# Performance work log

Measured on AMD Instinct MI355X. Metric: run time of the kernel, lower is better.

The kernel has to match this reference:

```python
import jax, jax.numpy as jnp
import numpy as np

GROUPS = 8
EPS = 1e-5
PERM_IN = {'x': (0, 2, 4, 1, 3), 'y': (0, 2, 3, 1, 4), 'seq': (0, 3, 4, 1, 2)}
PERM_OUT = {'x': (0, 3, 1, 4, 2), 'y': (0, 3, 1, 2, 4), 'seq': (0, 3, 4, 1, 2)}


def bn_train(x, gamma, beta, axis=1):
    """Training-mode batch norm: normalize over all axes except `axis`."""
    axes = tuple(i for i in range(x.ndim) if i != axis)
    mean = x.mean(axes, keepdims=True)
    var = x.var(axes, keepdims=True)
    shp = [1] * x.ndim
    shp[axis] = x.shape[axis]
    return (x - mean) * jax.lax.rsqrt(var + EPS) * gamma.reshape(shp) + beta.reshape(shp)


def axial_attn(x, qkv_w, gq, bq, gs, bs, go, bo, direction):
    # x: (N, C, seq, H, W)
    x = jnp.transpose(x, PERM_IN[direction])
    N, seq, W, C, H = x.shape
    B = N * seq * W
    xf = x.reshape(B, C, H)
    # 1x1 conv1d qkv projection + BN over channels
    qkv = jnp.einsum('oc,bch->boh', qkv_w, xf)            # (B, 2C, H)
    qkv = bn_train(qkv, gq, bq, axis=1)
    gp = C // GROUPS                                       # group_planes
    qkv = qkv.reshape(B, GROUPS, 2 * gp, H)
    q = qkv[:, :, : gp // 2]
    k = qkv[:, :, gp // 2: gp]
    v = qkv[:, :, gp:]
    qk = jnp.einsum('bgci,bgcj->bgij', q, k)               # (B, g, H, H)
    qk = bn_train(qk, gs, bs, axis=1)
    sim = jax.nn.softmax(qk, axis=3)
    sv = jnp.einsum('bgij,bgcj->bgci', sim, v)             # (B, g, gp, H)
    sv = bn_train(sv.reshape(B, C, H), go, bo, axis=1)
    out = sv.reshape(N, seq, W, C, H)
    return jnp.transpose(out, PERM_OUT[direction])


def setup_inputs() -> dict:
    key = jax.random.key(0)
    ks = jax.random.split(key, 4)
    N, C_in, seq, H, W = 2, 128, 16, 56, 56
    width = 64
    x = jax.random.normal(ks[0], (N, C_in, seq, H, W), jnp.float32)
    cd_w = jax.random.normal(ks[1], (width, C_in), jnp.float32) * (1.0 / np.sqrt(C_in))
    qkv_w = jax.random.normal(ks[2], (3, 2 * width, width), jnp.float32) * (1.0 / np.sqrt(width))
    cu_w = jax.random.normal(ks[3], (2 * width, width), jnp.float32) * (1.0 / np.sqrt(width))
    return {
        'x': x,
        'cd_w': cd_w,
        'bn1_g': jnp.ones((width,), jnp.float32),
        'bn1_b': jnp.zeros((width,), jnp.float32),
        'qkv_w': qkv_w,
        'bnq_g': jnp.ones((3, 2 * width), jnp.float32),
        'bnq_b': jnp.zeros((3, 2 * width), jnp.float32),
        'bns_g': jnp.ones((3, GROUPS), jnp.float32),
        'bns_b': jnp.zeros((3, GROUPS), jnp.float32),
        'bno_g': jnp.ones((3, width), jnp.float32),
        'bno_b': jnp.zeros((3, width), jnp.float32),
        'cu_w': cu_w,
        'bn2_g': jnp.ones((2 * width,), jnp.float32),
        'bn2_b': jnp.zeros((2 * width,), jnp.float32),
    }


def reference(x, cd_w, bn1_g, bn1_b, qkv_w, bnq_g, bnq_b, bns_g, bns_b,
              bno_g, bno_b, cu_w, bn2_g, bn2_b):
    identity = x
    out = jnp.einsum('oc,ncshw->noshw', cd_w, x)           # conv_down (1x1)
    out = jax.nn.relu(bn_train(out, bn1_g, bn1_b, axis=1))
    for i, d in enumerate(('x', 'y', 'seq')):              # height, width, seq axial passes
        out = axial_attn(out, qkv_w[i], bnq_g[i], bnq_b[i], bns_g[i], bns_b[i],
                         bno_g[i], bno_b[i], d)
    out = jax.nn.relu(out)
    out = jnp.einsum('oc,ncshw->noshw', cu_w, out)         # conv_up (1x1)
    out = bn_train(out, bn2_g, bn2_b, axis=1)
    return jax.nn.relu(out + identity)
```

## Files before the change

### kernel.cpp

```cpp
#include <hip/hip_runtime.h>

constexpr int SP = 16*56*56;
constexpr int P  = 2*SP;
constexpr float EPSV = 1e-5f;

constexpr size_t SZ_A   = (size_t)2*64*SP;
constexpr size_t OFF_A  = 0;
constexpr size_t OFF_C  = SZ_A;
constexpr size_t OFF_ST = OFF_C + SZ_A;
constexpr size_t OFF_P1 = 0;
constexpr size_t OFF_P2 = 65536;

__global__ void __launch_bounds__(256) kern_down(
    const float* __restrict__ x, const float* __restrict__ w,
    float* __restrict__ A, float* __restrict__ st)
{
  __shared__ float xs[128*64];
  __shared__ float wt[64*129];
  __shared__ float ssum[64], ssq[64];
  const int t = threadIdx.x;
  if (t < 64) { ssum[t] = 0.f; ssq[t] = 0.f; }
  const int p0 = blockIdx.x * 64;
  const int n = p0 / SP, rem = p0 % SP;
  const float* xb = x + (size_t)n*128*SP + rem;
  for (int e = t; e < 128*64; e += 256) {
    int c = e >> 6, p = e & 63;
    xs[e] = xb[(size_t)c*SP + p];
  }
  for (int e = t; e < 64*128; e += 256) {
    int o = e >> 7, c = e & 127;
    wt[o*129 + c] = w[e];
  }
  __syncthreads();
  const int og = t & 15, pg = t >> 4;
  float acc[4][4] = {};
  for (int c = 0; c < 128; ++c) {
    float xv[4], wv[4];
    #pragma unroll
    for (int j = 0; j < 4; ++j) xv[j] = xs[c*64 + pg*4 + j];
    #pragma unroll
    for (int i = 0; i < 4; ++i) wv[i] = wt[(og + 16*i)*129 + c];
    #pragma unroll
    for (int i = 0; i < 4; ++i) {
      #pragma unroll
      for (int j = 0; j < 4; ++j) acc[i][j] = fmaf(wv[i], xv[j], acc[i][j]);
    }
  }
  float* Ab = A + (size_t)n*64*SP + rem;
  #pragma unroll
  for (int i = 0; i < 4; ++i) {
    const int o = og + 16*i;
    float s1 = 0.f, s2 = 0.f;
    #pragma unroll
    for (int j = 0; j < 4; ++j) { float v = acc[i][j]; s1 += v; s2 += v*v; }
    float4 v4 = make_float4(acc[i][0], acc[i][1], acc[i][2], acc[i][3]);
    *reinterpret_cast<float4*>(Ab + (size_t)o*SP + pg*4) = v4;
    atomicAdd(&ssum[o], s1);
    atomicAdd(&ssq[o], s2);
  }
  __syncthreads();
  if (t < 64) { atomicAdd(&st[t], ssum[t]); atomicAdd(&st[64+t], ssq[t]); }
}

__global__ void __launch_bounds__(256) kern_up(
    const float* __restrict__ A, const float* __restrict__ w,
    float* __restrict__ U, float* __restrict__ st)
{
  __shared__ float xs[64*64];
  __shared__ float wt[128*65];
  __shared__ float ssum[128], ssq[128];
  const int t = threadIdx.x;
  if (t < 128) { ssum[t]=0.f; ssq[t]=0.f; }
  const int p0 = blockIdx.x*64;
  const int n = p0/SP, rem = p0%SP;
  const float* Ab = A + (size_t)n*64*SP + rem;
  for (int e = t; e < 64*64; e += 256) {
    int c = e >> 6, p = e & 63;
    xs[e] = fmaxf(Ab[(size_t)c*SP + p], 0.f);
  }
  for (int e = t; e < 128*64; e += 256) {
    int o = e >> 6, c = e & 63;
    wt[o*65 + c] = w[e];
  }
  __syncthreads();
  const int og = t & 31, pg = t >> 5;
  float acc[4][8] = {};
  for (int c = 0; c < 64; ++c) {
    float xv[8];
    #pragma unroll
    for (int j = 0; j < 8; ++j) xv[j] = xs[c*64 + pg*8 + j];
    #pragma unroll
    for (int i = 0; i < 4; ++i) {
      float wv = wt[(og + 32*i)*65 + c];
      #pragma unroll
      for (int j = 0; j < 8; ++j) acc[i][j] = fmaf(wv, xv[j], acc[i][j]);
    }
  }
  float* Ub = U + (size_t)n*128*SP + rem;
  #pragma unroll
  for (int i = 0; i < 4; ++i) {
    const int o = og + 32*i;
    float s1=0.f, s2=0.f;
    #pragma unroll
    for (int j = 0; j < 8; ++j) { float v = acc[i][j]; s1 += v; s2 += v*v; }
    float4 a = make_float4(acc[i][0],acc[i][1],acc[i][2],acc[i][3]);
    float4 b = make_float4(acc[i][4],acc[i][5],acc[i][6],acc[i][7]);
    *reinterpret_cast<float4*>(Ub + (size_t)o*SP + pg*8)     = a;
    *reinterpret_cast<float4*>(Ub + (size_t)o*SP + pg*8 + 4) = b;
    atomicAdd(&ssum[o], s1); atomicAdd(&ssq[o], s2);
  }
  __syncthreads();
  if (t < 128) { atomicAdd(&st[t], ssum[t]); atomicAdd(&st[128+t], ssq[t]); }
}

template<int DIR, bool FIRST>
__global__ void __launch_bounds__(256) kern_qkv(
    const float* __restrict__ A, const float* __restrict__ w,
    const float* __restrict__ sc1, const float* __restrict__ sh1,
    float* __restrict__ Bq, float* __restrict__ st)
{
  constexpr int H = 56;
  constexpr int SHJ = H/8;
  __shared__ float xs[64*H];
  __shared__ float wt[128*65];
  __shared__ float ssum[128], ssq[128];
  const int t = threadIdx.x;
  if (t < 128) { ssum[t]=0.f; ssq[t]=0.f; }
  const int b = blockIdx.x;
  size_t base; int strT;
  if (DIR == 0)      { int n=b/896,  r=b%896,  s=r/56, ww=r%56; base=(size_t)n*64*SP + s*3136 + ww;    strT=56;   }
  else               { int n=b/896,  r=b%896,  s=r/56, y=r%56;  base=(size_t)n*64*SP + s*3136 + y*56;  strT=1;    }
  for (int e = t; e < 64*H; e += 256) {
    int c = e / H, j = e % H;
    float v = A[base + (size_t)c*SP + (size_t)j*strT];
    if (FIRST) v = fmaxf(fmaf(v, sc1[c], sh1[c]), 0.f);
    xs[e] = v;
  }
  for (int e = t; e < 128*64; e += 256) { int o=e>>6, c=e&63; wt[o*65+c]=w[e]; }
  __syncthreads();
  const int og = t & 31, hg = t >> 5;
  float acc[4][SHJ];
  #pragma unroll
  for (int i=0;i<4;++i) {
    #pragma unroll
    for (int j=0;j<SHJ;++j) acc[i][j]=0.f;
  }
  for (int c = 0; c < 64; ++c) {
    float xv[SHJ];
    #pragma unroll
    for (int j = 0; j < SHJ; ++j) xv[j] = xs[c*H + hg*SHJ + j];
    #pragma unroll
    for (int i = 0; i < 4; ++i) {
      float wv = wt[(og + 32*i)*65 + c];
      #pragma unroll
      for (int j = 0; j < SHJ; ++j) acc[i][j] = fmaf(wv, xv[j], acc[i][j]);
    }
  }
  float* ob = Bq + (size_t)b*128*H;
  #pragma unroll
  for (int i = 0; i < 4; ++i) {
    const int o = og + 32*i;
    float s1=0.f, s2=0.f;
    #pragma unroll
    for (int j = 0; j < SHJ; ++j) {
      float v = acc[i][j];
      ob[o*H + hg*SHJ + j] = v;
      s1 += v; s2 += v*v;
    }
    atomicAdd(&ssum[o], s1); atomicAdd(&ssq[o], s2);
  }
  __syncthreads();
  if (t < 128) { atomicAdd(&st[t], ssum[t]); atomicAdd(&st[128+t], ssq[t]); }
}

__global__ void __launch_bounds__(256) kern_qkv2(
    const float* __restrict__ A, const float* __restrict__ w,
    float* __restrict__ Bq, float* __restrict__ st)
{
  __shared__ float xs[64*64];
  __shared__ float wt[128*65];
  __shared__ float ssum[128], ssq[128];
  const int t = threadIdx.x;
  if (t < 128) { ssum[t]=0.f; ssq[t]=0.f; }
  const int b = blockIdx.x;
  const int n = b/784, r = b%784, y = r/14, w4 = (r%14)*4;
  const float* Ab = A + (size_t)n*64*SP + y*56 + w4;
  for (int e = t; e < 1024; e += 256) {
    int c = e >> 4, s = e & 15;
    float4 v = *reinterpret_cast<const float4*>(Ab + (size_t)c*SP + s*3136);
    xs[c*64 + s]      = v.x;
    xs[c*64 + 16 + s] = v.y;
    xs[c*64 + 32 + s] = v.z;
    xs[c*64 + 48 + s] = v.w;
  }
  for (int e = t; e < 128*64; e += 256) { int o=e>>6, c=e&63; wt[o*65+c]=w[e]; }
  __syncthreads();
  const int og = t & 31, cg = t >> 5;
  float acc[4][8] = {};
  for (int c = 0; c < 64; ++c) {
    float xv[8];
    #pragma unroll
    for (int j = 0; j < 8; ++j) xv[j] = xs[c*64 + cg*8 + j];
    #pragma unroll
    for (int i = 0; i < 4; ++i) {
      float wv = wt[(og + 32*i)*65 + c];
      #pragma unroll
      for (int j = 0; j < 8; ++j) acc[i][j] = fmaf(wv, xv[j], acc[i][j]);
    }
  }
  const size_t b0 = (size_t)n*3136 + (size_t)y*56 + w4;
  #pragma unroll
  for (int i = 0; i < 4; ++i) {
    const int o = og + 32*i;
    float s1=0.f, s2=0.f;
    #pragma unroll
    for (int j = 0; j < 8; ++j) {
      int col = cg*8 + j, wl = col >> 4, s = col & 15;
      float v = acc[i][j];
      Bq[(b0 + wl)*2048 + o*16 + s] = v;
      s1 += v; s2 += v*v;
    }
    atomicAdd(&ssum[o], s1); atomicAdd(&ssq[o], s2);
  }
  __syncthreads();
  if (t < 128) { atomicAdd(&st[t], ssum[t]); atomicAdd(&st[128+t], ssq[t]); }
}

__global__ void __launch_bounds__(256) kern_red(
    const float* __restrict__ part, float* __restrict__ stout, int nb, int stride)
{
  const int ch = blockIdx.x;
  float s = 0.f;
  for (int i = threadIdx.x; i < nb; i += 256) s += part[(size_t)i*stride + ch];
  #pragma unroll
  for (int off = 32; off >= 1; off >>= 1) s += __shfl_xor(s, off);
  __shared__ float red[4];
  if ((threadIdx.x & 63) == 0) red[threadIdx.x >> 6] = s;
  __syncthreads();
  if (threadIdx.x == 0) stout[ch] = red[0] + red[1] + red[2] + red[3];
}

template<int H>
__global__ void __launch_bounds__(256) kern_pass1(
    const float* __restrict__ Bq, const float* __restrict__ qsc,
    const float* __restrict__ qsh, float* __restrict__ part)
{
  constexpr int PW = (H==16) ? 4 : 1;
  const int t = threadIdx.x;
  const int wave = t >> 6, lane = t & 63;
  const int sub = (PW==1) ? 0 : (lane >> 4);
  const int i = (PW==1) ? lane : (lane & 15);
  __shared__ float kls[4][4*H*PW];
  __shared__ float bs[16];
  if (t < 16) bs[t] = 0.f;
  float* klw = kls[wave];
  const int pair0 = (blockIdx.x*4 + wave)*PW;
  for (int e = lane; e < 4*H*PW; e += 64) {
    int sp = e / (4*H), r = e % (4*H);
    int c = r / H, j = r % H;
    int pr = pair0 + sp, bb = pr >> 3, g = pr & 7;
    int o = g*16 + 4 + c;
    klw[e] = fmaf(Bq[((size_t)bb*128 + o)*H + j], qsc[o], qsh[o]);
  }
  __syncthreads();
  const int pr = pair0 + sub, bb = pr >> 3, g = pr & 7;
  const float* kp = klw + sub*4*H;
  const bool act = (i < H);
  float q[4];
  #pragma unroll
  for (int c = 0; c < 4; ++c) {
    int o = g*16 + c;
    q[c] = act ? fmaf(Bq[((size_t)bb*128 + o)*H + i], qsc[o], qsh[o]) : 0.f;
  }
  float s1 = 0.f, s2 = 0.f;
  #pragma unroll
  for (int j = 0; j < H; ++j) {
    float s = q[0]*kp[j] + q[1]*kp[H+j] + q[2]*kp[2*H+j] + q[3]*kp[3*H+j];
    s1 += s; s2 += s*s;
  }
  #pragma unroll
  for (int off = (PW==1?32:8); off >= 1; off >>= 1) {
    s1 += __shfl_xor(s1, off);
    s2 += __shfl_xor(s2, off);
  }
  if ((lane & (PW==1?63:15)) == 0) { atomicAdd(&bs[g], s1); atomicAdd(&bs[8+g], s2); }
  __syncthreads();
  if (t < 16) part[(size_t)blockIdx.x*16 + t] = bs[t];
}

template<int H>
__global__ void __launch_bounds__(256) kern_attn(
    const float* __restrict__ Bq, const float* __restrict__ qsc,
    const float* __restrict__ qsh, const float* __restrict__ ssc,
    float* __restrict__ C, float* __restrict__ part)
{
  constexpr int PW = (H==16) ? 4 : 1;
  const int t = threadIdx.x;
  const int wave = t >> 6, lane = t & 63;
  const int sub = (PW==1) ? 0 : (lane >> 4);
  const int i = (PW==1) ? lane : (lane & 15);
  __shared__ float kv[4][12*H*PW];
  __shared__ float bsum[64], bsq[64];
  if (t < 64) { bsum[t] = 0.f; bsq[t] = 0.f; }
  float* kvw = kv[wave];
  const int pair0 = (blockIdx.x*4 + wave)*PW;
  for (int e = lane; e < 12*H*PW; e += 64) {
    int sp = e / (12*H), r = e % (12*H);
    int c = r / H, j = r % H;
    int pr = pair0 + sp, bb = pr >> 3, g = pr & 7;
    int o = g*16 + 4 + c;
    kvw[e] = fmaf(Bq[((size_t)bb*128 + o)*H + j], qsc[o], qsh[o]);
  }
  __syncthreads();
  const int pr = pair0 + sub, bb = pr >> 3, g = pr & 7;
  const float* kp = kvw + sub*12*H;
  const bool act = (i < H);
  float q[4];
  #pragma unroll
  for (int c = 0; c < 4; ++c) {
    int o = g*16 + c;
    q[c] = act ? fmaf(Bq[((size_t)bb*128 + o)*H + i], qsc[o], qsh[o]) : 0.f;
  }
  const float As = ssc[g];
  float m = -3.4e38f;
  for (int j = 0; j < H; ++j) {
    float s = As * (q[0]*kp[j] + q[1]*kp[H+j] + q[2]*kp[2*H+j] + q[3]*kp[3*H+j]);
    m = fmaxf(m, s);
  }
  float den = 0.f;
  float acc[8] = {};
  for (int j = 0; j < H; ++j) {
    float s = As * (q[0]*kp[j] + q[1]*kp[H+j] + q[2]*kp[2*H+j] + q[3]*kp[3*H+j]);
    float e = __expf(s - m);
    den += e;
    #pragma unroll
    for (int c = 0; c < 8; ++c) acc[c] = fmaf(e, kp[(4+c)*H + j], acc[c]);
  }
  const float inv = 1.f/den;
  #pragma unroll
  for (int c = 0; c < 8; ++c) {
    float vv = act ? acc[c]*inv : 0.f;
    if (act) C[((size_t)bb*64 + g*8 + c)*H + i] = vv;
    float s1 = vv, s2 = vv*vv;
    #pragma unroll
    for (int off = (PW==1?32:8); off >= 1; off >>= 1) {
      s1 += __shfl_xor(s1, off);
      s2 += __shfl_xor(s2, off);
    }
    if ((lane & (PW==1?63:15)) == 0) { atomicAdd(&bsum[g*8+c], s1); atomicAdd(&bsq[g*8+c], s2); }
  }
  __syncthreads();
  if (t < 64) {
    part[(size_t)blockIdx.x*128 + t]      = bsum[t];
    part[(size_t)blockIdx.x*128 + 64 + t] = bsq[t];
  }
}

__global__ void __launch_bounds__(256) kern_scat0(
    const float* __restrict__ C, const float* __restrict__ osc,
    const float* __restrict__ osh, float* __restrict__ A)
{
  __shared__ float tile[56*57];
  const int bid = blockIdx.x;
  const int c = bid & 63, s = (bid >> 6) & 15, n = bid >> 10;
  const float sc = osc[c], sh = osh[c];
  const size_t cb = ((size_t)(n*16+s)*56)*3584 + c*56;
  for (int e = threadIdx.x; e < 3136; e += 256) {
    int w = e/56, h = e%56;
    tile[w*57+h] = C[cb + (size_t)w*3584 + h];
  }
  __syncthreads();
  const size_t ab = ((size_t)(n*64+c)*16+s)*3136;
  for (int e = threadIdx.x; e < 3136; e += 256) {
    int h = e/56, w = e%56;
    A[ab + e] = fmaf(tile[w*57+h], sc, sh);
  }
}

__global__ void __launch_bounds__(256) kern_scat1(
    const float* __restrict__ C, const float* __restrict__ osc,
    const float* __restrict__ osh, float* __restrict__ A)
{
  const int e = blockIdx.x*256 + threadIdx.x;
  if (e >= 1792*64*56) return;
  const int w = e % 56, c = (e/56) & 63, b = e / (56*64);
  const int n = b/896, r = b%896, s = r/56, y = r%56;
  A[((size_t)(n*64+c)*16+s)*3136 + y*56 + w] = fmaf(C[e], osc[c], osh[c]);
}

__global__ void __launch_bounds__(256) kern_scat2(
    const float* __restrict__ C, const float* __restrict__ osc,
    const float* __restrict__ osh, float* __restrict__ A)
{
  __shared__ float tile[56*17];
  const int bid = blockIdx.x;
  const int y = bid % 56, c = (bid/56) & 63, n = bid / 3584;
  const float sc = osc[c], sh = osh[c];
  const size_t cb = ((size_t)(n*56+y)*56)*1024 + c*16;
  for (int e = threadIdx.x; e < 896; e += 256) {
    int w = e >> 4, s = e & 15;
    tile[w*17+s] = C[cb + (size_t)w*1024 + s];
  }
  __syncthreads();
  const size_t ab = (size_t)(n*64+c)*16*3136 + y*56;
  for (int e = threadIdx.x; e < 896; e += 256) {
    int s = e/56, w = e%56;
    A[ab + (size_t)s*3136 + w] = fmaf(tile[w*17+s], sc, sh);
  }
}

__global__ void kern_fin_bn(float* __restrict__ st, const float* __restrict__ g,
                            const float* __restrict__ b, int nch, float invc)
{
  const int t = threadIdx.x;
  if (t < nch) {
    float mean = st[t]*invc;
    float var  = st[nch+t]*invc - mean*mean;
    float sc   = g[t]*rsqrtf(var + EPSV);
    st[2*nch+t] = sc;
    st[3*nch+t] = b[t] - mean*sc;
  }
}

__global__ void __launch_bounds__(256) kern_final(
    float* __restrict__ U, const float* __restrict__ x,
    const float* __restrict__ sc, const float* __restrict__ sh,
    float* __restrict__ out)
{
  const int idx = blockIdx.x*256 + threadIdx.x;
  if (idx >= P*128/4) return;
  const int e = idx*4;
  const int o = (e / SP) & 127;
  float4 u  = *reinterpret_cast<const float4*>(U + e);
  float4 xv = *reinterpret_cast<const float4*>(x + e);
  const float s = sc[o], h = sh[o];
  float4 r;
  r.x = fmaxf(fmaf(u.x, s, h) + xv.x, 0.f);
  r.y = fmaxf(fmaf(u.y, s, h) + xv.y, 0.f);
  r.z = fmaxf(fmaf(u.z, s, h) + xv.z, 0.f);
  r.w = fmaxf(fmaf(u.w, s, h) + xv.w, 0.f);
  *reinterpret_cast<float4*>(out + e) = r;
}

extern "C" void kernel_launch(void* const* d_in, const int* in_sizes, int n_in,
                              void* d_out, int out_size, void* d_ws, size_t ws_size,
                              hipStream_t stream)
{
  const float* x    = (const float*)d_in[0];
  const float* cdw  = (const float*)d_in[1];
  const float* bn1g = (const float*)d_in[2];
  const float* bn1b = (const float*)d_in[3];
  const float* qkvw = (const float*)d_in[4];
  const float* bnqg = (const float*)d_in[5];
  const float* bnqb = (const float*)d_in[6];
  const float* bnsg = (const float*)d_in[7];
  const float* bnsb = (const float*)d_in[8];
  const float* bnog = (const float*)d_in[9];
  const float* bnob = (const float*)d_in[10];
  const float* cuw  = (const float*)d_in[11];
  const float* bn2g = (const float*)d_in[12];
  const float* bn2b = (const float*)d_in[13];
  float* out = (float*)d_out;
  float* ws  = (float*)d_ws;

  float* A   = ws + OFF_A;
  float* C   = ws + OFF_C;
  float* st  = ws + OFF_ST;
  float* Pp1 = ws + OFF_P1;
  float* Pp2 = ws + OFF_P2;
  float* Bq  = out;

  hipMemsetAsync(st, 0, 4096*sizeof(float), stream);

  const float invP = 1.f/100352.f;

  kern_down<<<P/64, 256, 0, stream>>>(x, cdw, A, st);
  kern_fin_bn<<<1, 128, 0, stream>>>(st, bn1g, bn1b, 64, invP);

  {
    float* stq = st + 256; float* sts = stq + 512; float* sto = stq + 544;
    kern_qkv<0,true><<<1792, 256, 0, stream>>>(A, qkvw, st+128, st+192, Bq, stq);
    kern_fin_bn<<<1, 128, 0, stream>>>(stq, bnqg, bnqb, 128, invP);
    kern_pass1<56><<<3584, 256, 0, stream>>>(Bq, stq+256, stq+384, Pp1);
    kern_red<<<16, 256, 0, stream>>>(Pp1, sts, 3584, 16);
    kern_fin_bn<<<1, 128, 0, stream>>>(sts, bnsg, bnsb, 8, 1.f/5619712.f);
    kern_attn<56><<<3584, 256, 0, stream>>>(Bq, stq+256, stq+384, sts+16, C, Pp2);
    kern_red<<<128, 256, 0, stream>>>(Pp2, sto, 3584, 128);
    kern_fin_bn<<<1, 128, 0, stream>>>(sto, bnog, bnob, 64, invP);
    kern_scat0<<<2048, 256, 0, stream>>>(C, sto+128, sto+192, A);
  }
  {
    float* stq = st + 256 + 1024; float* sts = stq + 512; float* sto = stq + 544;
    kern_qkv<1,false><<<1792, 256, 0, stream>>>(A, qkvw+8192, st, st, Bq, stq);
    kern_fin_bn<<<1, 128, 0, stream>>>(stq, bnqg+128, bnqb+128, 128, invP);
    kern_pass1<56><<<3584, 256, 0, stream>>>(Bq, stq+256, stq+384, Pp1);
    kern_red<<<16, 256, 0, stream>>>(Pp1, sts, 3584, 16);
    kern_fin_bn<<<1, 128, 0, stream>>>(sts, bnsg+8, bnsb+8, 8, 1.f/5619712.f);
    kern_attn<56><<<3584, 256, 0, stream>>>(Bq, stq+256, stq+384, sts+16, C, Pp2);
    kern_red<<<128, 256, 0, stream>>>(Pp2, sto, 3584, 128);
    kern_fin_bn<<<1, 128, 0, stream>>>(sto, bnog+64, bnob+64, 64, invP);
    kern_scat1<<<25088, 256, 0, stream>>>(C, sto+128, sto+192, A);
  }
  {
    float* stq = st + 256 + 2048; float* sts = stq + 512; float* sto = stq + 544;
    kern_qkv2<<<1568, 256, 0, stream>>>(A, qkvw+16384, Bq, stq);
    kern_fin_bn<<<1, 128, 0, stream>>>(stq, bnqg+256, bnqb+256, 128, invP);
    kern_pass1<16><<<3136, 256, 0, stream>>>(Bq, stq+256, stq+384, Pp1);
    kern_red<<<16, 256, 0, stream>>>(Pp1, sts, 3136, 16);
    kern_fin_bn<<<1, 128, 0, stream>>>(sts, bnsg+16, bnsb+16, 8, 1.f/1605632.f);
    kern_attn<16><<<3136, 256, 0, stream>>>(Bq, stq+256, stq+384, sts+16, C, Pp2);
    kern_red<<<128, 256, 0, stream>>>(Pp2, sto, 3136, 128);
    kern_fin_bn<<<1, 128, 0, stream>>>(sto, bnog+128, bnob+128, 64, invP);
    kern_scat2<<<7168, 256, 0, stream>>>(C, sto+128, sto+192, A);
  }

  float* st2 = st + 3328;
  kern_up<<<P/64, 256, 0, stream>>>(A, cuw, Bq, st2);
  kern_fin_bn<<<1, 128, 0, stream>>>(st2, bn2g, bn2b, 128, invP);
  kern_final<<<P*128/4/256, 256, 0, stream>>>(Bq, x, st2+256, st2+384, out);
}
```

Before: 667.1 us.

## Vectorize tile loads, pre-transpose x-pass input, fuse partial reduce with BN finalize

Global-to-shared loads in the down, up and qkv kernels now use float4 instead of scalar loads. For the first axial pass, a new transpose kernel rewrites A so each H/W plane is transposed, which lets one qkv kernel read contiguous rows instead of strided columns. The separate partial-sum reduction and BN finalize launches are merged into one kernel that writes scale and shift directly, removing several small launches. The cost is an extra full read and write of A for the transpose, and it relies on C being free as scratch at that point.

```diff
diff --git a/kernel.cpp b/kernel.cpp
--- a/kernel.cpp
+++ b/kernel.cpp
@@ -23,13 +23,15 @@
   const int p0 = blockIdx.x * 64;
   const int n = p0 / SP, rem = p0 % SP;
   const float* xb = x + (size_t)n*128*SP + rem;
-  for (int e = t; e < 128*64; e += 256) {
-    int c = e >> 6, p = e & 63;
-    xs[e] = xb[(size_t)c*SP + p];
-  }
-  for (int e = t; e < 64*128; e += 256) {
-    int o = e >> 7, c = e & 127;
-    wt[o*129 + c] = w[e];
+  for (int e4 = t; e4 < 128*16; e4 += 256) {
+    int c = e4 >> 4, p4 = (e4 & 15)*4;
+    float4 v = *reinterpret_cast<const float4*>(xb + (size_t)c*SP + p4);
+    *reinterpret_cast<float4*>(&xs[c*64 + p4]) = v;
+  }
+  for (int e4 = t; e4 < 64*32; e4 += 256) {
+    int o = e4 >> 5, c4 = (e4 & 31)*4;
+    float4 v = *reinterpret_cast<const float4*>(w + o*128 + c4);
+    *reinterpret_cast<float4*>(&wt[o*129 + c4]) = v;
   }
   __syncthreads();
   const int og = t & 15, pg = t >> 4;
@@ -62,6 +64,25 @@
   if (t < 64) { atomicAdd(&st[t], ssum[t]); atomicAdd(&st[64+t], ssq[t]); }
 }
 
+__global__ void __launch_bounds__(256) kern_tr(
+    const float* __restrict__ A, float* __restrict__ At)
+{
+  __shared__ float tile[56*57];
+  const size_t base = (size_t)blockIdx.x*3136;
+  for (int e4 = threadIdx.x; e4 < 784; e4 += 256) {
+    int e = e4*4, h = e/56, w = e%56;
+    float4 v = *reinterpret_cast<const float4*>(A + base + e);
+    tile[w*57+h] = v.x; tile[(w+1)*57+h] = v.y;
+    tile[(w+2)*57+h] = v.z; tile[(w+3)*57+h] = v.w;
+  }
+  __syncthreads();
+  for (int e4 = threadIdx.x; e4 < 784; e4 += 256) {
+    int e = e4*4, w = e/56, h = e%56;
+    float4 v = make_float4(tile[w*57+h], tile[w*57+h+1], tile[w*57+h+2], tile[w*57+h+3]);
+    *reinterpret_cast<float4*>(At + base + e) = v;
+  }
+}
+
 __global__ void __launch_bounds__(256) kern_up(
     const float* __restrict__ A, const float* __restrict__ w,
     float* __restrict__ U, float* __restrict__ st)
@@ -74,13 +95,16 @@
   const int p0 = blockIdx.x*64;
   const int n = p0/SP, rem = p0%SP;
   const float* Ab = A + (size_t)n*64*SP + rem;
-  for (int e = t; e < 64*64; e += 256) {
-    int c = e >> 6, p = e & 63;
-    xs[e] = fmaxf(Ab[(size_t)c*SP + p], 0.f);
-  }
-  for (int e = t; e < 128*64; e += 256) {
-    int o = e >> 6, c = e & 63;
-    wt[o*65 + c] = w[e];
+  for (int e4 = t; e4 < 64*16; e4 += 256) {
+    int c = e4 >> 4, p4 = (e4 & 15)*4;
+    float4 v = *reinterpret_cast<const float4*>(Ab + (size_t)c*SP + p4);
+    v.x = fmaxf(v.x, 0.f); v.y = fmaxf(v.y, 0.f); v.z = fmaxf(v.z, 0.f); v.w = fmaxf(v.w, 0.f);
+    *reinterpret_cast<float4*>(&xs[c*64 + p4]) = v;
+  }
+  for (int e4 = t; e4 < 128*16; e4 += 256) {
+    int o = e4 >> 4, c4 = (e4 & 15)*4;
+    float4 v = *reinterpret_cast<const float4*>(w + o*64 + c4);
+    *reinterpret_cast<float4*>(&wt[o*65 + c4]) = v;
   }
   __syncthreads();
   const int og = t & 31, pg = t >> 5;
@@ -113,47 +137,49 @@
   if (t < 128) { atomicAdd(&st[t], ssum[t]); atomicAdd(&st[128+t], ssq[t]); }
 }
 
-template<int DIR, bool FIRST>
+template<bool FIRST>
 __global__ void __launch_bounds__(256) kern_qkv(
-    const float* __restrict__ A, const float* __restrict__ w,
+    const float* __restrict__ src, const float* __restrict__ w,
     const float* __restrict__ sc1, const float* __restrict__ sh1,
     float* __restrict__ Bq, float* __restrict__ st)
 {
   constexpr int H = 56;
-  constexpr int SHJ = H/8;
   __shared__ float xs[64*H];
   __shared__ float wt[128*65];
   __shared__ float ssum[128], ssq[128];
   const int t = threadIdx.x;
   if (t < 128) { ssum[t]=0.f; ssq[t]=0.f; }
   const int b = blockIdx.x;
-  size_t base; int strT;
-  if (DIR == 0)      { int n=b/896,  r=b%896,  s=r/56, ww=r%56; base=(size_t)n*64*SP + s*3136 + ww;    strT=56;   }
-  else               { int n=b/896,  r=b%896,  s=r/56, y=r%56;  base=(size_t)n*64*SP + s*3136 + y*56;  strT=1;    }
-  for (int e = t; e < 64*H; e += 256) {
-    int c = e / H, j = e % H;
-    float v = A[base + (size_t)c*SP + (size_t)j*strT];
-    if (FIRST) v = fmaxf(fmaf(v, sc1[c], sh1[c]), 0.f);
-    xs[e] = v;
-  }
-  for (int e = t; e < 128*64; e += 256) { int o=e>>6, c=e&63; wt[o*65+c]=w[e]; }
+  const int n = b/896, r = b%896, s = r/56, q = r%56;
+  const size_t base = (size_t)n*64*SP + s*3136 + q*56;
+  for (int e4 = t; e4 < 64*14; e4 += 256) {
+    int c = e4/14, j4 = (e4%14)*4;
+    float4 v = *reinterpret_cast<const float4*>(src + base + (size_t)c*SP + j4);
+    if (FIRST) {
+      float sc = sc1[c], sh = sh1[c];
+      v.x = fmaxf(fmaf(v.x, sc, sh), 0.f); v.y = fmaxf(fmaf(v.y, sc, sh), 0.f);
+      v.z = fmaxf(fmaf(v.z, sc, sh), 0.f); v.w = fmaxf(fmaf(v.w, sc, sh), 0.f);
+    }
+    xs[c*H + j4]   = v.x; xs[c*H + j4+1] = v.y;
+    xs[c*H + j4+2] = v.z; xs[c*H + j4+3] = v.w;
+  }
+  for (int e4 = t; e4 < 128*16; e4 += 256) {
+    int o = e4 >> 4, c4 = (e4 & 15)*4;
+    float4 v = *reinterpret_cast<const float4*>(w + o*64 + c4);
+    *reinterpret_cast<float4*>(&wt[o*65 + c4]) = v;
+  }
   __syncthreads();
   const int og = t & 31, hg = t >> 5;
-  float acc[4][SHJ];
-  #pragma unroll
-  for (int i=0;i<4;++i) {
-    #pragma unroll
-    for (int j=0;j<SHJ;++j) acc[i][j]=0.f;
-  }
+  float acc[4][7] = {};
   for (int c = 0; c < 64; ++c) {
-    float xv[SHJ];
-    #pragma unroll
-    for (int j = 0; j < SHJ; ++j) xv[j] = xs[c*H + hg*SHJ + j];
+    float xv[7];
+    #pragma unroll
+    for (int j = 0; j < 7; ++j) xv[j] = xs[c*H + hg*7 + j];
     #pragma unroll
     for (int i = 0; i < 4; ++i) {
       float wv = wt[(og + 32*i)*65 + c];
       #pragma unroll
-      for (int j = 0; j < SHJ; ++j) acc[i][j] = fmaf(wv, xv[j], acc[i][j]);
+      for (int j = 0; j < 7; ++j) acc[i][j] = fmaf(wv, xv[j], acc[i][j]);
     }
   }
   float* ob = Bq + (size_t)b*128*H;
@@ -162,9 +188,9 @@
     const int o = og + 32*i;
     float s1=0.f, s2=0.f;
     #pragma unroll
-    for (int j = 0; j < SHJ; ++j) {
+    for (int j = 0; j < 7; ++j) {
       float v = acc[i][j];
-      ob[o*H + hg*SHJ + j] = v;
+      ob[o*H + hg*7 + j] = v;
       s1 += v; s2 += v*v;
     }
     atomicAdd(&ssum[o], s1); atomicAdd(&ssq[o], s2);
@@ -193,7 +219,11 @@
     xs[c*64 + 32 + s] = v.z;
     xs[c*64 + 48 + s] = v.w;
   }
-  for (int e = t; e < 128*64; e += 256) { int o=e>>6, c=e&63; wt[o*65+c]=w[e]; }
+  for (int e4 = t; e4 < 128*16; e4 += 256) {
+    int o = e4 >> 4, c4 = (e4 & 15)*4;
+    float4 v = *reinterpret_cast<const float4*>(w + o*64 + c4);
+    *reinterpret_cast<float4*>(&wt[o*65 + c4]) = v;
+  }
   __syncthreads();
   const int og = t & 31, cg = t >> 5;
   float acc[4][8] = {};
@@ -226,18 +256,30 @@
   if (t < 128) { atomicAdd(&st[t], ssum[t]); atomicAdd(&st[128+t], ssq[t]); }
 }
 
-__global__ void __launch_bounds__(256) kern_red(
-    const float* __restrict__ part, float* __restrict__ stout, int nb, int stride)
+__global__ void __launch_bounds__(256) kern_redfin(
+    const float* __restrict__ part, const float* __restrict__ g,
+    const float* __restrict__ b, float* __restrict__ scsh,
+    int nb, int nch, float invc)
 {
   const int ch = blockIdx.x;
-  float s = 0.f;
-  for (int i = threadIdx.x; i < nb; i += 256) s += part[(size_t)i*stride + ch];
-  #pragma unroll
-  for (int off = 32; off >= 1; off >>= 1) s += __shfl_xor(s, off);
-  __shared__ float red[4];
-  if ((threadIdx.x & 63) == 0) red[threadIdx.x >> 6] = s;
-  __syncthreads();
-  if (threadIdx.x == 0) stout[ch] = red[0] + red[1] + red[2] + red[3];
+  const int t = threadIdx.x;
+  float s1 = 0.f, s2 = 0.f;
+  for (int i = t; i < nb; i += 256) {
+    s1 += part[(size_t)i*2*nch + ch];
+    s2 += part[(size_t)i*2*nch + nch + ch];
+  }
+  #pragma unroll
+  for (int off = 32; off >= 1; off >>= 1) { s1 += __shfl_xor(s1, off); s2 += __shfl_xor(s2, off); }
+  __shared__ float r1[4], r2[4];
+  if ((t & 63) == 0) { r1[t>>6] = s1; r2[t>>6] = s2; }
+  __syncthreads();
+  if (t == 0) {
+    float S1 = r1[0]+r1[1]+r1[2]+r1[3], S2 = r2[0]+r2[1]+r2[2]+r2[3];
+    float mean = S1*invc, var = S2*invc - mean*mean;
+    float sc = g[ch]*rsqrtf(var + EPSV);
+    scsh[ch] = sc;
+    scsh[nch + ch] = b[ch] - mean*sc;
+  }
 }
 
 template<int H>
@@ -479,39 +521,34 @@
 
   {
     float* stq = st + 256; float* sts = stq + 512; float* sto = stq + 544;
-    kern_qkv<0,true><<<1792, 256, 0, stream>>>(A, qkvw, st+128, st+192, Bq, stq);
+    kern_tr<<<2048, 256, 0, stream>>>(A, C);
+    kern_qkv<true><<<1792, 256, 0, stream>>>(C, qkvw, st+128, st+192, Bq, stq);
     kern_fin_bn<<<1, 128, 0, stream>>>(stq, bnqg, bnqb, 128, invP);
     kern_pass1<56><<<3584, 256, 0, stream>>>(Bq, stq+256, stq+384, Pp1);
-    kern_red<<<16, 256, 0, stream>>>(Pp1, sts, 3584, 16);
-    kern_fin_bn<<<1, 128, 0, stream>>>(sts, bnsg, bnsb, 8, 1.f/5619712.f);
-    kern_attn<56><<<3584, 256, 0, stream>>>(Bq, stq+256, stq+384, sts+16, C, Pp2);
-    kern_red<<<128, 256, 0, stream>>>(Pp2, sto, 3584, 128);
-    kern_fin_bn<<<1, 128, 0, stream>>>(sto, bnog, bnob, 64, invP);
-    kern_scat0<<<2048, 256, 0, stream>>>(C, sto+128, sto+192, A);
+    kern_redfin<<<8, 256, 0, stream>>>(Pp1, bnsg, bnsb, sts, 3584, 8, 1.f/5619712.f);
+    kern_attn<56><<<3584, 256, 0, stream>>>(Bq, stq+256, stq+384, sts, C, Pp2);
+    kern_redfin<<<64, 256, 0, stream>>>(Pp2, bnog, bnob, sto, 3584, 64, invP);
+    kern_scat0<<<2048, 256, 0, stream>>>(C, sto, sto+64, A);
   }
   {
     float* stq = st + 256 + 1024; float* sts = stq + 512; float* sto = stq + 544;
-    kern_qkv<1,false><<<1792, 256, 0, stream>>>(A, qkvw+8192, st, st, Bq, stq);
+    kern_qkv<false><<<1792, 256, 0, stream>>>(A, qkvw+8192, st, st, Bq, stq);
     kern_fin_bn<<<1, 128, 0, stream>>>(stq, bnqg+128, bnqb+128, 128, invP);
     kern_pass1<56><<<3584, 256, 0, stream>>>(Bq, stq+256, stq+384, Pp1);
-    kern_red<<<16, 256, 0, stream>>>(Pp1, sts, 3584, 16);
-    kern_fin_bn<<<1, 128, 0, stream>>>(sts, bnsg+8, bnsb+8, 8, 1.f/5619712.f);
-    kern_attn<56><<<3584, 256, 0, stream>>>(Bq, stq+256, stq+384, sts+16, C, Pp2);
-    kern_red<<<128, 256, 0, stream>>>(Pp2, sto, 3584, 128);
-    kern_fin_bn<<<1, 128, 0, stream>>>(sto, bnog+64, bnob+64, 64, invP);
-    kern_scat1<<<25088, 256, 0, stream>>>(C, sto+128, sto+192, A);
+    kern_redfin<<<8, 256, 0, stream>>>(Pp1, bnsg+8, bnsb+8, sts, 3584, 8, 1.f/5619712.f);
+    kern_attn<56><<<3584, 256, 0, stream>>>(Bq, stq+256, stq+384, sts, C, Pp2);
+    kern_redfin<<<64, 256, 0, stream>>>(Pp2, bnog+64, bnob+64, sto, 3584, 64, invP);
+    kern_scat1<<<25088, 256, 0, stream>>>(C, sto, sto+64, A);
   }
   {
     float* stq = st + 256 + 2048; float* sts = stq + 512; float* sto = stq + 544;
     kern_qkv2<<<1568, 256, 0, stream>>>(A, qkvw+16384, Bq, stq);
     kern_fin_bn<<<1, 128, 0, stream>>>(stq, bnqg+256, bnqb+256, 128, invP);
     kern_pass1<16><<<3136, 256, 0, stream>>>(Bq, stq+256, stq+384, Pp1);
-    kern_red<<<16, 256, 0, stream>>>(Pp1, sts, 3136, 16);
-    kern_fin_bn<<<1, 128, 0, stream>>>(sts, bnsg+16, bnsb+16, 8, 1.f/1605632.f);
-    kern_attn<16><<<3136, 256, 0, stream>>>(Bq, stq+256, stq+384, sts+16, C, Pp2);
-    kern_red<<<128, 256, 0, stream>>>(Pp2, sto, 3136, 128);
-    kern_fin_bn<<<1, 128, 0, stream>>>(sto, bnog+128, bnob+128, 64, invP);
-    kern_scat2<<<7168, 256, 0, stream>>>(C, sto+128, sto+192, A);
+    kern_redfin<<<8, 256, 0, stream>>>(Pp1, bnsg+16, bnsb+16, sts, 3136, 8, 1.f/1605632.f);
+    kern_attn<16><<<3136, 256, 0, stream>>>(Bq, stq+256, stq+384, sts, C, Pp2);
+    kern_redfin<<<64, 256, 0, stream>>>(Pp2, bnog+128, bnob+128, sto, 3136, 64, invP);
+    kern_scat2<<<7168, 256, 0, stream>>>(C, sto, sto+64, A);
   }
 
   float* st2 = st + 3328;
```

After: 661.1 us. About the same (-0.9%).
